# Kernel optimization log

Hardware: AMD Instinct MI355X
Metric: run time of the kernel (lower is better)

## Reference

```python
import jax, jax.numpy as jnp
import numpy as np

B, T, N, C_IN, C_OUT, CHEB_K, ST_EMB = 8, 12, 2048, 64, 64, 2, 64


def setup_inputs() -> dict:
    key = jax.random.key(0)
    ks = jax.random.split(key, 9)
    inv = 1.0 / np.sqrt(ST_EMB)
    return {
        "x": jax.random.normal(ks[0], (B, T, N, C_IN), dtype=jnp.float32),
        "adj": jax.random.uniform(ks[1], (N, N), dtype=jnp.float32),
        "st_emb": jax.random.normal(ks[2], (T, 1, ST_EMB), dtype=jnp.float32),
        "weights": jax.random.normal(ks[3], (CHEB_K, C_IN, C_OUT), dtype=jnp.float32) * 0.02,
        "bias": jax.random.normal(ks[4], (C_OUT,), dtype=jnp.float32) * 0.02,
        "W1": jax.random.uniform(ks[5], (ST_EMB, 32), minval=-inv, maxval=inv, dtype=jnp.float32),
        "b1": jax.random.uniform(ks[6], (32,), minval=-inv, maxval=inv, dtype=jnp.float32),
        "W2": jax.random.uniform(ks[7], (32, 1), minval=-1/np.sqrt(32), maxval=1/np.sqrt(32), dtype=jnp.float32),
        "b2": jax.random.uniform(ks[8], (1,), minval=-1/np.sqrt(32), maxval=1/np.sqrt(32), dtype=jnp.float32),
    }


def reference(x, adj, st_emb, weights, bias, W1, b1, W2, b2):
    # lambda MLP: Linear -> ReLU -> Linear, then 1 + relu(.)
    h = jax.nn.relu(st_emb @ W1 + b1)            # [T,1,32]
    lam = 1.0 + jax.nn.relu(h @ W2 + b2)         # [T,1,1]
    c1 = (2.0 * lam - 2.0) / lam                 # [T,1,1] diagonal-scale coefficient
    c2 = 2.0 / lam                               # [T,1,1]
    # identity support einsum == per-time diagonal scaling of x
    x_g1 = c1[None] * x                          # [B,T,N,C]
    # adjacency support: scale factored out of the N x N contraction
    x_g2 = c2[None] * jnp.einsum('nm,btmc->btnc', adj, x)  # [B,T,N,C]
    x_g = jnp.stack([x_g1, x_g2], axis=3)        # [B,T,N,K,C]
    return jnp.einsum('btnki,kio->btno', x_g, weights) + bias
```

## Files before the change

kernel.cpp:

```cpp
#include <hip/hip_runtime.h>
#include <hip/hip_bf16.h>

#define B_ 8
#define T_ 12
#define N_ 2048
#define C_ 64
#define BM 128
#define BK 64

typedef __attribute__((ext_vector_type(4))) float f32x4;
typedef __attribute__((ext_vector_type(4))) __bf16 bf16x4;
typedef __attribute__((ext_vector_type(8))) __bf16 bf16x8;

#define GAS __attribute__((address_space(1)))
#define LAS __attribute__((address_space(3)))

static __device__ __forceinline__ void gld_lds16(const void* g, void* l) {
    __builtin_amdgcn_global_load_lds((const GAS void*)g, (LAS void*)l, 16, 0, 0);
}

#define WS_CBUF 0
#define WS_WTB  1024
#define WS_ADJB 32768
#define WS_P1T  (32768 + 8388608)
#define WS_P0S  (WS_P1T + 25165824)
#define WS_MID  ((size_t)WS_P0S)
#define WS_FULL ((size_t)WS_P0S + 25165824)

__global__ void lam_kernel(const float* __restrict__ st, const float* __restrict__ W1,
                           const float* __restrict__ b1, const float* __restrict__ W2,
                           const float* __restrict__ b2, float* __restrict__ cbuf) {
    const int t = threadIdx.x >> 5;
    const int h = threadIdx.x & 31;
    if (t >= T_) return;
    float acc = b1[h];
    #pragma unroll 8
    for (int e = 0; e < 64; ++e) acc += st[t * 64 + e] * W1[e * 32 + h];
    float hv = fmaxf(acc, 0.f) * W2[h];
    #pragma unroll
    for (int off = 16; off; off >>= 1) hv += __shfl_down(hv, off, 32);
    if (h == 0) {
        float lam = 1.f + fmaxf(hv + b2[0], 0.f);
        cbuf[t]      = 2.f - 2.f / lam;
        cbuf[T_ + t] = 2.f / lam;
    }
}

__global__ void lamw_kernel(const float* __restrict__ st, const float* __restrict__ W1,
                            const float* __restrict__ b1, const float* __restrict__ W2,
                            const float* __restrict__ b2, const float* __restrict__ weights,
                            float* __restrict__ cbuf, __bf16* __restrict__ WtB) {
    const int t = threadIdx.x >> 5;
    const int h = threadIdx.x & 31;
    if (t < T_) {
        float acc = b1[h];
        #pragma unroll 8
        for (int e = 0; e < 64; ++e) acc += st[t * 64 + e] * W1[e * 32 + h];
        float hv = fmaxf(acc, 0.f) * W2[h];
        #pragma unroll
        for (int off = 16; off; off >>= 1) hv += __shfl_down(hv, off, 32);
        if (h == 0) {
            float lam = 1.f + fmaxf(hv + b2[0], 0.f);
            cbuf[t]      = 2.f - 2.f / lam;
            cbuf[T_ + t] = 2.f / lam;
        }
    }
    for (int e = threadIdx.x; e < 64 * 128; e += 512) {
        int o = e >> 7, k = e & 127;
        float v = (k < 64) ? weights[4096 + k * 64 + o] : weights[(k - 64) * 64 + o];
        WtB[o * 128 + k] = (__bf16)v;
    }
}

template<bool FULLP>
__global__ __launch_bounds__(256, 4) void pcvt_kernel(
    const float* __restrict__ x, const float* __restrict__ adj,
    const __bf16* __restrict__ WtB, const float* __restrict__ cbuf,
    const float* __restrict__ bias, __bf16* __restrict__ adjb,
    __bf16* __restrict__ P1T, __bf16* __restrict__ P0S, float* __restrict__ out)
{
    const int bid = blockIdx.x;
    const int tid = threadIdx.x;
    if (bid >= 1536) {
        const size_t i = ((size_t)(bid - 1536) * 256 + tid) * 8;
        const float4 f0 = *(const float4*)&adj[i];
        const float4 f1 = *(const float4*)&adj[i + 4];
        bf16x8 h = { (__bf16)f0.x, (__bf16)f0.y, (__bf16)f0.z, (__bf16)f0.w,
                     (__bf16)f1.x, (__bf16)f1.y, (__bf16)f1.z, (__bf16)f1.w };
        *(bf16x8*)&adjb[i] = h;
        return;
    }
    __shared__ __align__(16) __bf16 T[64 * 128];
    char* TB = (char*)T;
    const int bt = bid >> 4, n0 = (bid & 15) * 128;
    const int l = tid & 63, w = tid >> 6;
    const int lr = l & 15, lk = l >> 4;
    const float c1 = cbuf[bt % T_];

    f32x4 p1[2][4] = {}, p0[2][4] = {};
    #pragma unroll
    for (int ks = 0; ks < 2; ++ks) {
        bf16x8 a[2];
        #pragma unroll
        for (int mi = 0; mi < 2; ++mi) {
            const float* xs = x + ((size_t)bt * N_ + n0 + w * 32 + mi * 16 + lr) * C_ + ks * 32 + lk * 8;
            float4 f0 = *(const float4*)xs;
            float4 f1 = *(const float4*)(xs + 4);
            a[mi] = { (__bf16)f0.x, (__bf16)f0.y, (__bf16)f0.z, (__bf16)f0.w,
                      (__bf16)f1.x, (__bf16)f1.y, (__bf16)f1.z, (__bf16)f1.w };
        }
        #pragma unroll
        for (int nj = 0; nj < 4; ++nj) {
            const __bf16* wb = WtB + (nj * 16 + lr) * 128 + ks * 32 + lk * 8;
            bf16x8 b1v = *(const bf16x8*)wb;
            bf16x8 b0v = *(const bf16x8*)(wb + 64);
            #pragma unroll
            for (int mi = 0; mi < 2; ++mi) {
                p1[mi][nj] = __builtin_amdgcn_mfma_f32_16x16x32_bf16(a[mi], b1v, p1[mi][nj], 0, 0, 0);
                p0[mi][nj] = __builtin_amdgcn_mfma_f32_16x16x32_bf16(a[mi], b0v, p0[mi][nj], 0, 0, 0);
            }
        }
    }
    #pragma unroll
    for (int nj = 0; nj < 4; ++nj) {
        const int o = nj * 16 + lr;
        const float bv = bias[o];
        #pragma unroll
        for (int mi = 0; mi < 2; ++mi)
            #pragma unroll
            for (int q = 0; q < 4; ++q) {
                const int row = w * 32 + mi * 16 + lk * 4 + q;
                const size_t idx = ((size_t)bt * N_ + n0 + row) * C_ + o;
                const float v = c1 * p0[mi][nj][q] + bv;
                if (FULLP) P0S[idx] = (__bf16)v; else out[idx] = v;
            }
    }
    #pragma unroll
    for (int nj = 0; nj < 4; ++nj) {
        const int o = nj * 16 + lr;
        #pragma unroll
        for (int mi = 0; mi < 2; ++mi)
            #pragma unroll
            for (int q = 0; q < 4; ++q) {
                const int row = w * 32 + mi * 16 + lk * 4 + q;
                *(__bf16*)(TB + o * 256 + ((row * 2) ^ ((o & 7) << 4))) = (__bf16)p1[mi][nj][q];
            }
    }
    __syncthreads();
    {
        const int o = tid >> 2, seg = tid & 3;
        __bf16* dst = P1T + ((size_t)bt * 64 + o) * N_ + n0 + seg * 32;
        #pragma unroll
        for (int i = 0; i < 4; ++i) {
            const int chunk = seg * 64 + i * 16;
            *(bf16x8*)(dst + i * 8) = *(const bf16x8*)(TB + o * 256 + (chunk ^ ((o & 7) << 4)));
        }
    }
}

template<bool FULLP>
__global__ __launch_bounds__(256, 3) void dgcn_main7(
    const __bf16* __restrict__ adjb, const __bf16* __restrict__ P1T,
    const __bf16* __restrict__ P0S, const float* __restrict__ cbuf,
    float* __restrict__ out)
{
    __shared__ __align__(16) __bf16 smem[16384];
    char* sb = (char*)smem;

    const int m0  = blockIdx.x * BM;
    const int btg = blockIdx.y;
    const int tid = threadIdx.x;
    const int l   = tid & 63, w = tid >> 6;
    const int wr  = w >> 1, wc = w & 1;
    const int lr  = l & 15, lk = l >> 4;

    const __bf16* srcA[4];
    const __bf16* srcB[4];
    #pragma unroll
    for (int i = 0; i < 4; ++i) {
        int s = (w * 4 + i) * 64 + l;
        int r = s >> 3, j = s & 7;
        srcA[i] = adjb + (size_t)(m0 + r) * N_ + 8 * (j ^ (r & 7));
        int bb = s >> 9, o = (s >> 3) & 63;
        srcB[i] = P1T + ((size_t)(btg * 2 + bb) * 64 + o) * N_ + 8 * (j ^ (o & 7));
    }

    f32x4 acc[4][4] = {};

    for (int kt = 0; kt < N_ / BK; ++kt) {
        __syncthreads();
        #pragma unroll
        for (int i = 0; i < 4; ++i) {
            gld_lds16(srcA[i], sb + (w * 4 + i) * 1024);
            gld_lds16(srcB[i], sb + 16384 + (w * 4 + i) * 1024);
            srcA[i] += BK;
            srcB[i] += BK;
        }
        __syncthreads();
        #pragma unroll
        for (int ks = 0; ks < 2; ++ks) {
            const int kb = ks * 64 + lk * 16;
            bf16x8 a[4];
            #pragma unroll
            for (int mi = 0; mi < 4; ++mi) {
                int rr = wr * 64 + mi * 16 + lr;
                a[mi] = *(const bf16x8*)(sb + rr * 128 + (kb ^ ((rr & 7) << 4)));
            }
            #pragma unroll
            for (int nj = 0; nj < 4; ++nj) {
                int cc = nj * 16 + lr;
                bf16x8 b = *(const bf16x8*)(sb + 16384 + wc * 8192 + cc * 128 + (kb ^ ((cc & 7) << 4)));
                #pragma unroll
                for (int mi = 0; mi < 4; ++mi)
                    acc[mi][nj] = __builtin_amdgcn_mfma_f32_16x16x32_bf16(a[mi], b, acc[mi][nj], 0, 0, 0);
            }
        }
    }

    const int btA = btg * 2 + wc;
    const float c2 = cbuf[T_ + (btA % T_)];
    #pragma unroll
    for (int nj = 0; nj < 4; ++nj) {
        const int o = nj * 16 + lr;
        #pragma unroll
        for (int mi = 0; mi < 4; ++mi)
            #pragma unroll
            for (int q = 0; q < 4; ++q) {
                const int row = wr * 64 + mi * 16 + lk * 4 + q;
                const size_t idx = ((size_t)btA * N_ + m0 + row) * C_ + o;
                const float p0v = FULLP ? (float)P0S[idx] : out[idx];
                out[idx] = c2 * acc[mi][nj][q] + p0v;
            }
    }
}

#define LDM 72
#define LDE 136
__global__ __launch_bounds__(256, 3) void dgcn_fb(
    const float* __restrict__ x, const float* __restrict__ adj,
    const float* __restrict__ weights, const float* __restrict__ bias,
    const float* __restrict__ cbuf, float* __restrict__ out)
{
    __shared__ __align__(16) __bf16 smem[BM * LDE];
    __shared__ __align__(16) __bf16 Wt[64 * LDE];
    __bf16* As = smem;
    __bf16* Bs = smem + BM * LDM;
    __bf16* E  = smem;

    const int mtile = blockIdx.x;
    const int bt    = blockIdx.y;
    const int tloc  = bt % T_;
    const int m0    = mtile * BM;
    const int tid   = threadIdx.x;
    const int lane  = tid & 63;
    const int w     = tid >> 6;

    const float c1 = cbuf[tloc];
    const float c2 = cbuf[T_ + tloc];
    const float* xbt = x + (size_t)bt * N_ * C_;

    for (int e = tid; e < 2 * 64 * 64; e += 256) {
        int kk = e >> 6, o = e & 63;
        float v = (kk < 64) ? weights[4096 + kk * 64 + o] : weights[(kk - 64) * 64 + o];
        Wt[o * LDE + kk] = (__bf16)v;
    }

    f32x4 acc[2][4] = {};
    const int c4 = tid & 15;
    const int rg = tid >> 4;
    const int lr = lane & 15;
    const int lk = lane >> 4;

    for (int kt = 0; kt < N_ / BK; ++kt) {
        const int k0 = kt * BK;
        __syncthreads();
        #pragma unroll
        for (int j = 0; j < 8; ++j) {
            const int r = rg + 16 * j;
            const float4 f = *(const float4*)&adj[(size_t)(m0 + r) * N_ + k0 + 4 * c4];
            bf16x4 h = { (__bf16)f.x, (__bf16)f.y, (__bf16)f.z, (__bf16)f.w };
            *(bf16x4*)&As[r * LDM + 4 * c4] = h;
        }
        #pragma unroll
        for (int j = 0; j < 4; ++j) {
            const int k  = (tid & 15) + 16 * j;
            const int c0 = 4 * (tid >> 4);
            const float4 f = *(const float4*)&xbt[(size_t)(k0 + k) * C_ + c0];
            Bs[(c0 + 0) * LDM + k] = (__bf16)f.x;
            Bs[(c0 + 1) * LDM + k] = (__bf16)f.y;
            Bs[(c0 + 2) * LDM + k] = (__bf16)f.z;
            Bs[(c0 + 3) * LDM + k] = (__bf16)f.w;
        }
        __syncthreads();
        #pragma unroll
        for (int ks = 0; ks < 2; ++ks) {
            bf16x8 a0 = *(const bf16x8*)&As[(w * 32 +  0 + lr) * LDM + ks * 32 + lk * 8];
            bf16x8 a1 = *(const bf16x8*)&As[(w * 32 + 16 + lr) * LDM + ks * 32 + lk * 8];
            #pragma unroll
            for (int nj = 0; nj < 4; ++nj) {
                bf16x8 b = *(const bf16x8*)&Bs[(nj * 16 + lr) * LDM + ks * 32 + lk * 8];
                acc[0][nj] = __builtin_amdgcn_mfma_f32_16x16x32_bf16(a0, b, acc[0][nj], 0, 0, 0);
                acc[1][nj] = __builtin_amdgcn_mfma_f32_16x16x32_bf16(a1, b, acc[1][nj], 0, 0, 0);
            }
        }
    }
    __syncthreads();

    #pragma unroll
    for (int j = 0; j < 8; ++j) {
        const int r = rg + 16 * j;
        const float4 f = *(const float4*)&xbt[(size_t)(m0 + r) * C_ + 4 * c4];
        bf16x4 h = { (__bf16)(c1 * f.x), (__bf16)(c1 * f.y), (__bf16)(c1 * f.z), (__bf16)(c1 * f.w) };
        *(bf16x4*)&E[r * LDE + 64 + 4 * c4] = h;
    }
    #pragma unroll
    for (int mi = 0; mi < 2; ++mi)
        #pragma unroll
        for (int nj = 0; nj < 4; ++nj)
            #pragma unroll
            for (int q = 0; q < 4; ++q) {
                const int row = w * 32 + mi * 16 + lk * 4 + q;
                const int col = nj * 16 + lr;
                E[row * LDE + col] = (__bf16)(c2 * acc[mi][nj][q]);
            }
    __syncthreads();

    f32x4 oacc[2][4] = {};
    #pragma unroll
    for (int ks = 0; ks < 4; ++ks) {
        bf16x8 a0 = *(const bf16x8*)&E[(w * 32 +  0 + lr) * LDE + ks * 32 + lk * 8];
        bf16x8 a1 = *(const bf16x8*)&E[(w * 32 + 16 + lr) * LDE + ks * 32 + lk * 8];
        #pragma unroll
        for (int nj = 0; nj < 4; ++nj) {
            bf16x8 bw = *(const bf16x8*)&Wt[(nj * 16 + lr) * LDE + ks * 32 + lk * 8];
            oacc[0][nj] = __builtin_amdgcn_mfma_f32_16x16x32_bf16(a0, bw, oacc[0][nj], 0, 0, 0);
            oacc[1][nj] = __builtin_amdgcn_mfma_f32_16x16x32_bf16(a1, bw, oacc[1][nj], 0, 0, 0);
        }
    }
    float* obt = out + (size_t)bt * N_ * C_;
    #pragma unroll
    for (int nj = 0; nj < 4; ++nj) {
        const float bv = bias[nj * 16 + lr];
        #pragma unroll
        for (int mi = 0; mi < 2; ++mi)
            #pragma unroll
            for (int q = 0; q < 4; ++q) {
                const int row = w * 32 + mi * 16 + lk * 4 + q;
                obt[(size_t)(m0 + row) * C_ + nj * 16 + lr] = oacc[mi][nj][q] + bv;
            }
    }
}

extern "C" void kernel_launch(void* const* d_in, const int* in_sizes, int n_in,
                              void* d_out, int out_size, void* d_ws, size_t ws_size,
                              hipStream_t stream) {
    const float* x       = (const float*)d_in[0];
    const float* adj     = (const float*)d_in[1];
    const float* st_emb  = (const float*)d_in[2];
    const float* weights = (const float*)d_in[3];
    const float* bias    = (const float*)d_in[4];
    const float* W1      = (const float*)d_in[5];
    const float* b1      = (const float*)d_in[6];
    const float* W2      = (const float*)d_in[7];
    const float* b2      = (const float*)d_in[8];
    float* out = (float*)d_out;
    char* ws = (char*)d_ws;
    float* cbuf = (float*)(ws + WS_CBUF);

    if (ws_size >= WS_MID) {
        __bf16* WtB  = (__bf16*)(ws + WS_WTB);
        __bf16* adjb = (__bf16*)(ws + WS_ADJB);
        __bf16* P1T  = (__bf16*)(ws + WS_P1T);
        __bf16* P0S  = (__bf16*)(ws + WS_P0S);
        lamw_kernel<<<1, 512, 0, stream>>>(st_emb, W1, b1, W2, b2, weights, cbuf, WtB);
        if (ws_size >= WS_FULL) {
            pcvt_kernel<true><<<3584, 256, 0, stream>>>(x, adj, WtB, cbuf, bias, adjb, P1T, P0S, out);
            dgcn_main7<true><<<dim3(N_ / BM, B_ * T_ / 2), 256, 0, stream>>>(adjb, P1T, P0S, cbuf, out);
        } else {
            pcvt_kernel<false><<<3584, 256, 0, stream>>>(x, adj, WtB, cbuf, bias, adjb, P1T, P0S, out);
            dgcn_main7<false><<<dim3(N_ / BM, B_ * T_ / 2), 256, 0, stream>>>(adjb, P1T, P0S, cbuf, out);
        }
    } else {
        lam_kernel<<<1, 384, 0, stream>>>(st_emb, W1, b1, W2, b2, cbuf);
        dgcn_fb<<<dim3(N_ / BM, B_ * T_), 256, 0, stream>>>(x, adj, weights, bias, cbuf, out);
    }
}
```

Measured before the change: 99.17 us.

## Triple-buffer LDS k-loop with BK=32 and XCD-aware block remapping

Replaces the single-buffered BK=64 main GEMM loop with a three-stage LDS ring at BK=32. Global-to-LDS loads for tile kt+2 are issued while tile kt is computed, with explicit vmcnt waits and raw s_barriers in place of two __syncthreads per iteration. The grid is also flattened to 1D and remapped so that blocks landing on the same XCD share bt groups, which should improve L2 reuse of the P1T panel. Costs are more LDS per block (48KB), which may lower occupancy, and finer k-steps that add barrier overhead.

```diff
diff --git a/kernel.cpp b/kernel.cpp
--- a/kernel.cpp
+++ b/kernel.cpp
@@ -6,7 +6,7 @@
 #define N_ 2048
 #define C_ 64
 #define BM 128
-#define BK 64
+#define BK 32
 
 typedef __attribute__((ext_vector_type(4))) float f32x4;
 typedef __attribute__((ext_vector_type(4))) __bf16 bf16x4;
@@ -159,62 +159,78 @@
 }
 
 template<bool FULLP>
-__global__ __launch_bounds__(256, 3) void dgcn_main7(
+__global__ __launch_bounds__(256, 3) void dgcn_main8(
     const __bf16* __restrict__ adjb, const __bf16* __restrict__ P1T,
     const __bf16* __restrict__ P0S, const float* __restrict__ cbuf,
     float* __restrict__ out)
 {
-    __shared__ __align__(16) __bf16 smem[16384];
+    __shared__ __align__(16) __bf16 smem[24576];
     char* sb = (char*)smem;
 
-    const int m0  = blockIdx.x * BM;
-    const int btg = blockIdx.y;
+    const int id   = blockIdx.x;
+    const int xcd  = id & 7;
+    const int wi   = id >> 3;
+    const int btg  = xcd * 6 + (wi >> 4);
+    const int m0   = (wi & 15) * BM;
+
     const int tid = threadIdx.x;
     const int l   = tid & 63, w = tid >> 6;
     const int wr  = w >> 1, wc = w & 1;
     const int lr  = l & 15, lk = l >> 4;
 
-    const __bf16* srcA[4];
-    const __bf16* srcB[4];
-    #pragma unroll
-    for (int i = 0; i < 4; ++i) {
-        int s = (w * 4 + i) * 64 + l;
-        int r = s >> 3, j = s & 7;
-        srcA[i] = adjb + (size_t)(m0 + r) * N_ + 8 * (j ^ (r & 7));
-        int bb = s >> 9, o = (s >> 3) & 63;
-        srcB[i] = P1T + ((size_t)(btg * 2 + bb) * 64 + o) * N_ + 8 * (j ^ (o & 7));
+    const __bf16* srcA[2];
+    const __bf16* srcB[2];
+    #pragma unroll
+    for (int i = 0; i < 2; ++i) {
+        int s = (w * 2 + i) * 64 + l;
+        int r = s >> 2, j = s & 3;
+        srcA[i] = adjb + (size_t)(m0 + r) * N_ + 8 * (j ^ ((r >> 1) & 3));
+        int bb = s >> 8, o = (s >> 2) & 63;
+        srcB[i] = P1T + ((size_t)(btg * 2 + bb) * 64 + o) * N_ + 8 * (j ^ ((o >> 1) & 3));
     }
 
     f32x4 acc[4][4] = {};
 
-    for (int kt = 0; kt < N_ / BK; ++kt) {
-        __syncthreads();
-        #pragma unroll
-        for (int i = 0; i < 4; ++i) {
-            gld_lds16(srcA[i], sb + (w * 4 + i) * 1024);
-            gld_lds16(srcB[i], sb + 16384 + (w * 4 + i) * 1024);
+    auto STAGE = [&]__attribute__((always_inline))(char* buf) {
+        #pragma unroll
+        for (int i = 0; i < 2; ++i) {
+            gld_lds16(srcA[i], buf + (w * 2 + i) * 1024);
+            gld_lds16(srcB[i], buf + 8192 + (w * 2 + i) * 1024);
             srcA[i] += BK;
             srcB[i] += BK;
         }
-        __syncthreads();
-        #pragma unroll
-        for (int ks = 0; ks < 2; ++ks) {
-            const int kb = ks * 64 + lk * 16;
-            bf16x8 a[4];
-            #pragma unroll
-            for (int mi = 0; mi < 4; ++mi) {
-                int rr = wr * 64 + mi * 16 + lr;
-                a[mi] = *(const bf16x8*)(sb + rr * 128 + (kb ^ ((rr & 7) << 4)));
-            }
-            #pragma unroll
-            for (int nj = 0; nj < 4; ++nj) {
-                int cc = nj * 16 + lr;
-                bf16x8 b = *(const bf16x8*)(sb + 16384 + wc * 8192 + cc * 128 + (kb ^ ((cc & 7) << 4)));
-                #pragma unroll
-                for (int mi = 0; mi < 4; ++mi)
-                    acc[mi][nj] = __builtin_amdgcn_mfma_f32_16x16x32_bf16(a[mi], b, acc[mi][nj], 0, 0, 0);
-            }
-        }
+    };
+    auto COMPUTE = [&]__attribute__((always_inline))(const char* base) {
+        bf16x8 a[4];
+        #pragma unroll
+        for (int mi = 0; mi < 4; ++mi) {
+            int rr = wr * 64 + mi * 16 + lr;
+            a[mi] = *(const bf16x8*)(base + rr * 64 + 16 * (lk ^ ((rr >> 1) & 3)));
+        }
+        #pragma unroll
+        for (int nj = 0; nj < 4; ++nj) {
+            int cc = nj * 16 + lr;
+            bf16x8 b = *(const bf16x8*)(base + 8192 + wc * 4096 + cc * 64 + 16 * (lk ^ ((cc >> 1) & 3)));
+            #pragma unroll
+            for (int mi = 0; mi < 4; ++mi)
+                acc[mi][nj] = __builtin_amdgcn_mfma_f32_16x16x32_bf16(a[mi], b, acc[mi][nj], 0, 0, 0);
+        }
+    };
+
+    const int NT = N_ / BK;
+    STAGE(sb);
+    STAGE(sb + 16384);
+
+    #pragma unroll 1
+    for (int kt = 0; kt < NT; ++kt) {
+        if (kt == NT - 1) asm volatile("s_waitcnt vmcnt(0)" ::: "memory");
+        else              asm volatile("s_waitcnt vmcnt(4)" ::: "memory");
+        __builtin_amdgcn_sched_barrier(0);
+        __builtin_amdgcn_s_barrier();
+        char* base = sb + (kt % 3) * 16384;
+        COMPUTE(base);
+        __builtin_amdgcn_s_barrier();
+        if (kt + 2 < NT) STAGE(sb + ((kt + 2) % 3) * 16384);
     }
 
     const int btA = btg * 2 + wc;
@@ -271,8 +287,8 @@
     const int lr = lane & 15;
     const int lk = lane >> 4;
 
-    for (int kt = 0; kt < N_ / BK; ++kt) {
-        const int k0 = kt * BK;
+    for (int kt = 0; kt < N_ / 64; ++kt) {
+        const int k0 = kt * 64;
         __syncthreads();
         #pragma unroll
         for (int j = 0; j < 8; ++j) {
@@ -375,10 +391,10 @@
         lamw_kernel<<<1, 512, 0, stream>>>(st_emb, W1, b1, W2, b2, weights, cbuf, WtB);
         if (ws_size >= WS_FULL) {
             pcvt_kernel<true><<<3584, 256, 0, stream>>>(x, adj, WtB, cbuf, bias, adjb, P1T, P0S, out);
-            dgcn_main7<true><<<dim3(N_ / BM, B_ * T_ / 2), 256, 0, stream>>>(adjb, P1T, P0S, cbuf, out);
+            dgcn_main8<true><<<768, 256, 0, stream>>>(adjb, P1T, P0S, cbuf, out);
         } else {
             pcvt_kernel<false><<<3584, 256, 0, stream>>>(x, adj, WtB, cbuf, bias, adjb, P1T, P0S, out);
-            dgcn_main7<false><<<dim3(N_ / BM, B_ * T_ / 2), 256, 0, stream>>>(adjb, P1T, P0S, cbuf, out);
+            dgcn_main8<false><<<768, 256, 0, stream>>>(adjb, P1T, P0S, cbuf, out);
         }
     } else {
         lam_kernel<<<1, 384, 0, stream>>>(st_emb, W1, b1, W2, b2, cbuf);
```

Result: slower. 105.8 us (+6.7%).

## Fuse identity-support GEMM into main kernel epilogue and drop P0S buffer

Applied to the files above, without the earlier changes.

The identity-support projection (c1*x@W0 + bias) is moved out of the pre-conversion kernel into the epilogue of the main adjacency GEMM. The main kernel reloads x, scales it by c1, runs extra MFMAs into the accumulator after scaling it by c2, then adds bias. This removes the bf16 P0S intermediate write and read. The adj-to-bf16 conversion is merged into the lambda/weight setup kernel, and the main grid is flattened with XCD-aware block-to-tile mapping. The cost is extra x reads and MFMA work in the main kernel, plus a launch-order dependency: pcvt now waits for the fused setup kernel, which also converts adj.

```diff
diff --git a/kernel.cpp b/kernel.cpp
--- a/kernel.cpp
+++ b/kernel.cpp
@@ -23,9 +23,7 @@
 #define WS_WTB  1024
 #define WS_ADJB 32768
 #define WS_P1T  (32768 + 8388608)
-#define WS_P0S  (WS_P1T + 25165824)
-#define WS_MID  ((size_t)WS_P0S)
-#define WS_FULL ((size_t)WS_P0S + 25165824)
+#define WS_MID  ((size_t)WS_P1T + 25165824)
 
 __global__ void lam_kernel(const float* __restrict__ st, const float* __restrict__ W1,
                            const float* __restrict__ b1, const float* __restrict__ W2,
@@ -46,43 +44,15 @@
     }
 }
 
-__global__ void lamw_kernel(const float* __restrict__ st, const float* __restrict__ W1,
-                            const float* __restrict__ b1, const float* __restrict__ W2,
-                            const float* __restrict__ b2, const float* __restrict__ weights,
-                            float* __restrict__ cbuf, __bf16* __restrict__ WtB) {
-    const int t = threadIdx.x >> 5;
-    const int h = threadIdx.x & 31;
-    if (t < T_) {
-        float acc = b1[h];
-        #pragma unroll 8
-        for (int e = 0; e < 64; ++e) acc += st[t * 64 + e] * W1[e * 32 + h];
-        float hv = fmaxf(acc, 0.f) * W2[h];
-        #pragma unroll
-        for (int off = 16; off; off >>= 1) hv += __shfl_down(hv, off, 32);
-        if (h == 0) {
-            float lam = 1.f + fmaxf(hv + b2[0], 0.f);
-            cbuf[t]      = 2.f - 2.f / lam;
-            cbuf[T_ + t] = 2.f / lam;
-        }
-    }
-    for (int e = threadIdx.x; e < 64 * 128; e += 512) {
-        int o = e >> 7, k = e & 127;
-        float v = (k < 64) ? weights[4096 + k * 64 + o] : weights[(k - 64) * 64 + o];
-        WtB[o * 128 + k] = (__bf16)v;
-    }
-}
-
-template<bool FULLP>
-__global__ __launch_bounds__(256, 4) void pcvt_kernel(
-    const float* __restrict__ x, const float* __restrict__ adj,
-    const __bf16* __restrict__ WtB, const float* __restrict__ cbuf,
-    const float* __restrict__ bias, __bf16* __restrict__ adjb,
-    __bf16* __restrict__ P1T, __bf16* __restrict__ P0S, float* __restrict__ out)
-{
+__global__ void lamw_adj_kernel(const float* __restrict__ st, const float* __restrict__ W1,
+                                const float* __restrict__ b1, const float* __restrict__ W2,
+                                const float* __restrict__ b2, const float* __restrict__ weights,
+                                const float* __restrict__ adj, float* __restrict__ cbuf,
+                                __bf16* __restrict__ WtB, __bf16* __restrict__ adjb) {
     const int bid = blockIdx.x;
     const int tid = threadIdx.x;
-    if (bid >= 1536) {
-        const size_t i = ((size_t)(bid - 1536) * 256 + tid) * 8;
+    if (bid > 0) {
+        const size_t i = ((size_t)(bid - 1) * 512 + tid) * 8;
         const float4 f0 = *(const float4*)&adj[i];
         const float4 f1 = *(const float4*)&adj[i + 4];
         bf16x8 h = { (__bf16)f0.x, (__bf16)f0.y, (__bf16)f0.z, (__bf16)f0.w,
@@ -90,14 +60,41 @@
         *(bf16x8*)&adjb[i] = h;
         return;
     }
+    const int t = tid >> 5;
+    const int h = tid & 31;
+    if (t < T_) {
+        float acc = b1[h];
+        #pragma unroll 8
+        for (int e = 0; e < 64; ++e) acc += st[t * 64 + e] * W1[e * 32 + h];
+        float hv = fmaxf(acc, 0.f) * W2[h];
+        #pragma unroll
+        for (int off = 16; off; off >>= 1) hv += __shfl_down(hv, off, 32);
+        if (h == 0) {
+            float lam = 1.f + fmaxf(hv + b2[0], 0.f);
+            cbuf[t]      = 2.f - 2.f / lam;
+            cbuf[T_ + t] = 2.f / lam;
+        }
+    }
+    for (int e = tid; e < 64 * 128; e += 512) {
+        int o = e >> 7, k = e & 127;
+        float v = (k < 64) ? weights[4096 + k * 64 + o] : weights[(k - 64) * 64 + o];
+        WtB[o * 128 + k] = (__bf16)v;
+    }
+}
+
+__global__ __launch_bounds__(256, 4) void pcvt_kernel(
+    const float* __restrict__ x, const __bf16* __restrict__ WtB,
+    __bf16* __restrict__ P1T)
+{
     __shared__ __align__(16) __bf16 T[64 * 128];
     char* TB = (char*)T;
+    const int bid = blockIdx.x;
+    const int tid = threadIdx.x;
     const int bt = bid >> 4, n0 = (bid & 15) * 128;
     const int l = tid & 63, w = tid >> 6;
     const int lr = l & 15, lk = l >> 4;
-    const float c1 = cbuf[bt % T_];
-
-    f32x4 p1[2][4] = {}, p0[2][4] = {};
+
+    f32x4 p1[2][4] = {};
     #pragma unroll
     for (int ks = 0; ks < 2; ++ks) {
         bf16x8 a[2];
@@ -111,29 +108,11 @@
         }
         #pragma unroll
         for (int nj = 0; nj < 4; ++nj) {
-            const __bf16* wb = WtB + (nj * 16 + lr) * 128 + ks * 32 + lk * 8;
-            bf16x8 b1v = *(const bf16x8*)wb;
-            bf16x8 b0v = *(const bf16x8*)(wb + 64);
-            #pragma unroll
-            for (int mi = 0; mi < 2; ++mi) {
+            bf16x8 b1v = *(const bf16x8*)(WtB + (nj * 16 + lr) * 128 + ks * 32 + lk * 8);
+            #pragma unroll
+            for (int mi = 0; mi < 2; ++mi)
                 p1[mi][nj] = __builtin_amdgcn_mfma_f32_16x16x32_bf16(a[mi], b1v, p1[mi][nj], 0, 0, 0);
-                p0[mi][nj] = __builtin_amdgcn_mfma_f32_16x16x32_bf16(a[mi], b0v, p0[mi][nj], 0, 0, 0);
-            }
-        }
-    }
-    #pragma unroll
-    for (int nj = 0; nj < 4; ++nj) {
-        const int o = nj * 16 + lr;
-        const float bv = bias[o];
-        #pragma unroll
-        for (int mi = 0; mi < 2; ++mi)
-            #pragma unroll
-            for (int q = 0; q < 4; ++q) {
-                const int row = w * 32 + mi * 16 + lk * 4 + q;
-                const size_t idx = ((size_t)bt * N_ + n0 + row) * C_ + o;
-                const float v = c1 * p0[mi][nj][q] + bv;
-                if (FULLP) P0S[idx] = (__bf16)v; else out[idx] = v;
-            }
+        }
     }
     #pragma unroll
     for (int nj = 0; nj < 4; ++nj) {
@@ -158,17 +137,21 @@
     }
 }
 
-template<bool FULLP>
-__global__ __launch_bounds__(256, 3) void dgcn_main7(
+__global__ __launch_bounds__(256, 3) void dgcn_main9(
     const __bf16* __restrict__ adjb, const __bf16* __restrict__ P1T,
-    const __bf16* __restrict__ P0S, const float* __restrict__ cbuf,
+    const float* __restrict__ x, const __bf16* __restrict__ WtB,
+    const float* __restrict__ bias, const float* __restrict__ cbuf,
     float* __restrict__ out)
 {
     __shared__ __align__(16) __bf16 smem[16384];
     char* sb = (char*)smem;
 
-    const int m0  = blockIdx.x * BM;
-    const int btg = blockIdx.y;
+    const int id  = blockIdx.x;
+    const int xcd = id & 7;
+    const int wi  = id >> 3;
+    const int btg = xcd * 6 + (wi >> 4);
+    const int m0  = (wi & 15) * BM;
+
     const int tid = threadIdx.x;
     const int l   = tid & 63, w = tid >> 6;
     const int wr  = w >> 1, wc = w & 1;
@@ -218,18 +201,46 @@
     }
 
     const int btA = btg * 2 + wc;
+    const float c1 = cbuf[btA % T_];
     const float c2 = cbuf[T_ + (btA % T_)];
+
+    bf16x8 xa[4][2];
+    #pragma unroll
+    for (int mi = 0; mi < 4; ++mi)
+        #pragma unroll
+        for (int ks = 0; ks < 2; ++ks) {
+            const float* xs = x + ((size_t)btA * N_ + m0 + wr * 64 + mi * 16 + lr) * C_ + ks * 32 + lk * 8;
+            float4 f0 = *(const float4*)xs;
+            float4 f1 = *(const float4*)(xs + 4);
+            xa[mi][ks] = { (__bf16)(c1 * f0.x), (__bf16)(c1 * f0.y),
+                           (__bf16)(c1 * f0.z), (__bf16)(c1 * f0.w),
+                           (__bf16)(c1 * f1.x), (__bf16)(c1 * f1.y),
+                           (__bf16)(c1 * f1.z), (__bf16)(c1 * f1.w) };
+        }
+    #pragma unroll
+    for (int mi = 0; mi < 4; ++mi)
+        #pragma unroll
+        for (int nj = 0; nj < 4; ++nj)
+            acc[mi][nj] *= c2;
+    #pragma unroll
+    for (int ks = 0; ks < 2; ++ks)
+        #pragma unroll
+        for (int nj = 0; nj < 4; ++nj) {
+            bf16x8 bw = *(const bf16x8*)(WtB + (nj * 16 + lr) * 128 + 64 + ks * 32 + lk * 8);
+            #pragma unroll
+            for (int mi = 0; mi < 4; ++mi)
+                acc[mi][nj] = __builtin_amdgcn_mfma_f32_16x16x32_bf16(xa[mi][ks], bw, acc[mi][nj], 0, 0, 0);
+        }
     #pragma unroll
     for (int nj = 0; nj < 4; ++nj) {
         const int o = nj * 16 + lr;
+        const float bv = bias[o];
         #pragma unroll
         for (int mi = 0; mi < 4; ++mi)
             #pragma unroll
             for (int q = 0; q < 4; ++q) {
                 const int row = wr * 64 + mi * 16 + lk * 4 + q;
-                const size_t idx = ((size_t)btA * N_ + m0 + row) * C_ + o;
-                const float p0v = FULLP ? (float)P0S[idx] : out[idx];
-                out[idx] = c2 * acc[mi][nj][q] + p0v;
+                out[((size_t)btA * N_ + m0 + row) * C_ + o] = acc[mi][nj][q] + bv;
             }
     }
 }
@@ -271,8 +282,8 @@
     const int lr = lane & 15;
     const int lk = lane >> 4;
 
-    for (int kt = 0; kt < N_ / BK; ++kt) {
-        const int k0 = kt * BK;
+    for (int kt = 0; kt < N_ / 64; ++kt) {
+        const int k0 = kt * 64;
         __syncthreads();
         #pragma unroll
         for (int j = 0; j < 8; ++j) {
@@ -371,15 +382,9 @@
         __bf16* WtB  = (__bf16*)(ws + WS_WTB);
         __bf16* adjb = (__bf16*)(ws + WS_ADJB);
         __bf16* P1T  = (__bf16*)(ws + WS_P1T);
-        __bf16* P0S  = (__bf16*)(ws + WS_P0S);
-        lamw_kernel<<<1, 512, 0, stream>>>(st_emb, W1, b1, W2, b2, weights, cbuf, WtB);
-        if (ws_size >= WS_FULL) {
-            pcvt_kernel<true><<<3584, 256, 0, stream>>>(x, adj, WtB, cbuf, bias, adjb, P1T, P0S, out);
-            dgcn_main7<true><<<dim3(N_ / BM, B_ * T_ / 2), 256, 0, stream>>>(adjb, P1T, P0S, cbuf, out);
-        } else {
-            pcvt_kernel<false><<<3584, 256, 0, stream>>>(x, adj, WtB, cbuf, bias, adjb, P1T, P0S, out);
-            dgcn_main7<false><<<dim3(N_ / BM, B_ * T_ / 2), 256, 0, stream>>>(adjb, P1T, P0S, cbuf, out);
-        }
+        lamw_adj_kernel<<<1025, 512, 0, stream>>>(st_emb, W1, b1, W2, b2, weights, adj, cbuf, WtB, adjb);
+        pcvt_kernel<<<1536, 256, 0, stream>>>(x, WtB, P1T);
+        dgcn_main9<<<768, 256, 0, stream>>>(adjb, P1T, x, WtB, bias, cbuf, out);
     } else {
         lam_kernel<<<1, 384, 0, stream>>>(st_emb, W1, b1, W2, b2, cbuf);
         dgcn_fb<<<dim3(N_ / BM, B_ * T_), 256, 0, stream>>>(x, adj, weights, bias, cbuf, out);
```

After: 96.60 us. 1.03x faster.
